# Optimization experiments

Hardware: AMD Instinct MI355X
Metric: run time of the kernel (lower is better)

## Reference

```python
import jax, jax.numpy as jnp
import numpy as np

C = 128
K = 8
B = 2
N = 8192


def setup_inputs() -> dict:
    key = jax.random.key(0)
    ks = jax.random.split(key, 7)
    feats = jax.random.normal(ks[0], (B, N, C), dtype=jnp.float32)
    coords = jax.random.normal(ks[1], (B, N, 3), dtype=jnp.float32)
    scale = 0.02
    Wq = jax.random.normal(ks[2], (C, C), dtype=jnp.float32) * scale
    Wk = jax.random.normal(ks[3], (C, C), dtype=jnp.float32) * scale
    Wv = jax.random.normal(ks[4], (C, C), dtype=jnp.float32) * scale
    Wo = jax.random.normal(ks[5], (C, C), dtype=jnp.float32) * scale
    log_gamma = jnp.log(jnp.float32(0.92))
    return {"feats": feats, "coords": coords, "Wq": Wq, "Wk": Wk,
            "Wv": Wv, "Wo": Wo, "log_gamma": log_gamma}


def _gather_neighbors(points, idx):
    # points: (B,N,C), idx: (B,N,K) -> (B,N,K,C)
    return jax.vmap(lambda p, i: p[i])(points, idx)


def _safe_norm(diff):
    # diff: (...,3) -> (...,) Euclidean norm with zero (not NaN) grad at 0
    d2 = jnp.sum(diff * diff, axis=-1)
    pos = d2 > 0
    return jnp.where(pos, jnp.sqrt(jnp.where(pos, d2, 1.0)), 0.0)


def reference(feats, coords, Wq, Wk, Wv, Wo, log_gamma):
    # nn.Linear(bias=False): y = x @ W.T with W of shape (out, in)
    q = feats @ Wq.T
    k = feats @ Wk.T
    v = feats @ Wv.T

    # KNN via dense pairwise Euclidean distance (mirrors torch.cdist + topk smallest)
    sq = jnp.sum(coords * coords, axis=-1)                      # (B,N)
    d2 = sq[:, :, None] + sq[:, None, :] - 2.0 * jnp.einsum('bnd,bmd->bnm', coords, coords)
    dist_full = jnp.sqrt(jnp.maximum(d2, 0.0))                  # (B,N,N)
    _, idx = jax.lax.top_k(-dist_full, K)                       # (B,N,K) nearest (incl. self)
    idx = jax.lax.stop_gradient(idx)

    k_neigh = _gather_neighbors(k, idx)                         # (B,N,K,C)
    v_neigh = _gather_neighbors(v, idx)                         # (B,N,K,C)
    coord_neigh = _gather_neighbors(coords, idx)                # (B,N,K,3)

    dist = _safe_norm(coords[:, :, None, :] - coord_neigh)      # (B,N,K)
    gamma_w = jnp.exp(log_gamma * dist)                         # (B,N,K)

    scores = jnp.einsum('bnc,bnkc->bnk', q, k_neigh) / (C ** 0.5)
    scores = scores * gamma_w
    weights = jax.nn.softmax(scores, axis=2)                    # (B,N,K)
    agg = jnp.einsum('bnk,bnkc->bnc', weights, v_neigh)         # (B,N,C)
    out = agg @ Wo.T
    return out
```

## Files before the change

kernel.cpp:

```cpp
#include <hip/hip_runtime.h>
#include <math.h>

#define C_DIM 128
#define KNN 8
#define NPTS 8192
#define M_TOTAL 16384
#define CHUNK 1024
#define SAMPLE 2048
#define CAND_CAP 96

typedef unsigned long long u64;

__global__ __launch_bounds__(256) void prep_and_transpose(
    const float* __restrict__ coords, float4* __restrict__ c4,
    const float* __restrict__ Wq, const float* __restrict__ Wk,
    const float* __restrict__ Wv, const float* __restrict__ Wo,
    float* __restrict__ Tq, float* __restrict__ Tk,
    float* __restrict__ Tv, float* __restrict__ To) {
  const int bid = blockIdx.x;
  const int t = threadIdx.x;
  if (bid < 64) {
    int g = bid * 256 + t;
    float x = coords[3 * g + 0];
    float y = coords[3 * g + 1];
    float z = coords[3 * g + 2];
    float s = fmaf(x, x, fmaf(y, y, z * z));
    c4[g] = make_float4(x, y, z, s);
  } else {
    int g = (bid - 64) * 256 + t;
    int mat = g >> 14;
    int j = g & 16383;
    int c = j >> 7, o = j & 127;
    const float* src = (mat == 0) ? Wq : (mat == 1) ? Wk : (mat == 2) ? Wv : Wo;
    float* dst = (mat == 0) ? Tq : (mat == 1) ? Tk : (mat == 2) ? Tv : To;
    dst[j] = src[o * C_DIM + c];
  }
}

__device__ __forceinline__ void stage_x64(
    float (*Xs)[132], const float* __restrict__ X, int row0, int t) {
  const float4* X4 = (const float4*)(X + (size_t)row0 * C_DIM);
  for (int i = t; i < 64 * 32; i += 256) {
    int r = i >> 5, c4i = i & 31;
    *(float4*)&Xs[r][c4i * 4] = X4[i];
  }
}

__global__ __launch_bounds__(256) void gemm_qkv(
    const float* __restrict__ X,
    const float* __restrict__ WTq, const float* __restrict__ WTk,
    const float* __restrict__ WTv,
    float* __restrict__ Yq, float* __restrict__ Yk, float* __restrict__ Yv) {
  __shared__ float Xs[64][132];
  __shared__ float Ws[3][16][64];
  const int t = threadIdx.x;
  const int row0 = (blockIdx.x >> 1) * 64;
  const int ob = (blockIdx.x & 1) * 64;

  stage_x64(Xs, X, row0, t);

  const int r0 = (t >> 4) * 4;
  const int o0l = (t & 15) * 4;
  const int wk = t >> 4;

  float aq[4][4], ak[4][4], av[4][4];
#pragma unroll
  for (int i = 0; i < 4; ++i)
#pragma unroll
    for (int j = 0; j < 4; ++j) { aq[i][j] = 0.f; ak[i][j] = 0.f; av[i][j] = 0.f; }

  for (int kc = 0; kc < C_DIM; kc += 16) {
    __syncthreads();
    {
      const size_t gsrc = (size_t)(kc + wk) * C_DIM + ob + o0l;
      *(float4*)&Ws[0][wk][o0l] = *(const float4*)&WTq[gsrc];
      *(float4*)&Ws[1][wk][o0l] = *(const float4*)&WTk[gsrc];
      *(float4*)&Ws[2][wk][o0l] = *(const float4*)&WTv[gsrc];
    }
    __syncthreads();

#pragma unroll
    for (int c = 0; c < 16; c += 4) {
      float xs[4][4];
#pragma unroll
      for (int i = 0; i < 4; ++i) {
        float4 xv = *(const float4*)&Xs[r0 + i][kc + c];
        xs[i][0] = xv.x; xs[i][1] = xv.y; xs[i][2] = xv.z; xs[i][3] = xv.w;
      }
#pragma unroll
      for (int cc = 0; cc < 4; ++cc) {
        float4 qa = *(const float4*)&Ws[0][c + cc][o0l];
        float4 ka = *(const float4*)&Ws[1][c + cc][o0l];
        float4 va = *(const float4*)&Ws[2][c + cc][o0l];
#pragma unroll
        for (int i = 0; i < 4; ++i) {
          float x = xs[i][cc];
          aq[i][0] = fmaf(x, qa.x, aq[i][0]); aq[i][1] = fmaf(x, qa.y, aq[i][1]);
          aq[i][2] = fmaf(x, qa.z, aq[i][2]); aq[i][3] = fmaf(x, qa.w, aq[i][3]);
          ak[i][0] = fmaf(x, ka.x, ak[i][0]); ak[i][1] = fmaf(x, ka.y, ak[i][1]);
          ak[i][2] = fmaf(x, ka.z, ak[i][2]); ak[i][3] = fmaf(x, ka.w, ak[i][3]);
          av[i][0] = fmaf(x, va.x, av[i][0]); av[i][1] = fmaf(x, va.y, av[i][1]);
          av[i][2] = fmaf(x, va.z, av[i][2]); av[i][3] = fmaf(x, va.w, av[i][3]);
        }
      }
    }
  }

#pragma unroll
  for (int i = 0; i < 4; ++i) {
    const size_t yoff = (size_t)(row0 + r0 + i) * C_DIM + ob + o0l;
    *(float4*)&Yq[yoff] = make_float4(aq[i][0], aq[i][1], aq[i][2], aq[i][3]);
    *(float4*)&Yk[yoff] = make_float4(ak[i][0], ak[i][1], ak[i][2], ak[i][3]);
    *(float4*)&Yv[yoff] = make_float4(av[i][0], av[i][1], av[i][2], av[i][3]);
  }
}

__global__ __launch_bounds__(256) void gemm_xwt(
    const float* __restrict__ X, const float* __restrict__ WT,
    float* __restrict__ Y) {
  __shared__ float Xs[64][132];
  __shared__ float Ws[16][64];
  const int t = threadIdx.x;
  const int row0 = (blockIdx.x >> 1) * 64;
  const int ob = (blockIdx.x & 1) * 64;

  stage_x64(Xs, X, row0, t);

  const int r0 = (t >> 4) * 4;
  const int o0l = (t & 15) * 4;
  const int wk = t >> 4;

  float acc[4][4];
#pragma unroll
  for (int i = 0; i < 4; ++i)
#pragma unroll
    for (int j = 0; j < 4; ++j) acc[i][j] = 0.0f;

  for (int kc = 0; kc < C_DIM; kc += 16) {
    __syncthreads();
    *(float4*)&Ws[wk][o0l] =
        *(const float4*)&WT[(size_t)(kc + wk) * C_DIM + ob + o0l];
    __syncthreads();

#pragma unroll
    for (int c = 0; c < 16; c += 4) {
      float xs[4][4];
#pragma unroll
      for (int i = 0; i < 4; ++i) {
        float4 xv = *(const float4*)&Xs[r0 + i][kc + c];
        xs[i][0] = xv.x; xs[i][1] = xv.y; xs[i][2] = xv.z; xs[i][3] = xv.w;
      }
#pragma unroll
      for (int cc = 0; cc < 4; ++cc) {
        float4 wa = *(const float4*)&Ws[c + cc][o0l];
#pragma unroll
        for (int i = 0; i < 4; ++i) {
          float x = xs[i][cc];
          acc[i][0] = fmaf(x, wa.x, acc[i][0]); acc[i][1] = fmaf(x, wa.y, acc[i][1]);
          acc[i][2] = fmaf(x, wa.z, acc[i][2]); acc[i][3] = fmaf(x, wa.w, acc[i][3]);
        }
      }
    }
  }

#pragma unroll
  for (int i = 0; i < 4; ++i) {
    float* yrow = Y + (size_t)(row0 + r0 + i) * C_DIM + ob + o0l;
    *(float4*)yrow = make_float4(acc[i][0], acc[i][1], acc[i][2], acc[i][3]);
  }
}

__device__ __forceinline__ u64 wave_min_u64(u64 x) {
#pragma unroll
  for (int off = 32; off > 0; off >>= 1) {
    u64 o = __shfl_xor(x, off, 64);
    x = (o < x) ? o : x;
  }
  return x;
}

__device__ __forceinline__ float wave_8th_of_top2(float u0, float u1) {
  float m = 0.0f;
#pragma unroll
  for (int r = 0; r < KNN; ++r) {
    m = u0;
#pragma unroll
    for (int off = 32; off > 0; off >>= 1) {
      float o = __shfl_xor(m, off, 64);
      m = fminf(m, o);
    }
    bool mine = (u0 == m);
    u0 = mine ? u1 : u0;
    u1 = mine ? INFINITY : u1;
  }
  return m;
}

__global__ __launch_bounds__(256) void knn_attn(
    const float4* __restrict__ c4,
    const float* __restrict__ q, const float* __restrict__ k,
    const float* __restrict__ v, const float* __restrict__ log_gamma_p,
    float* __restrict__ agg) {
  __shared__ float4 pts[CHUNK];
  __shared__ u64 cand[4][CAND_CAP];

  const int t = threadIdx.x;
  const int wave = t >> 6;
  const int lane = t & 63;
  const int qi = blockIdx.x * 4 + wave;
  const int b = qi >> 13;
  const int n = qi & (NPTS - 1);
  const int base = b * NPTS;

  const float4 qp = c4[base + n];
  const u64 lmask = (1ull << lane) - 1ull;

  float m1 = INFINITY, m2 = INFINITY;
  const float4* cb = c4 + base;
#pragma unroll 4
  for (int it = 0; it < SAMPLE / 64; ++it) {
    const float4 p = cb[it * 64 + lane];
    float dot = fmaf(qp.x, p.x, fmaf(qp.y, p.y, qp.z * p.z));
    float d2 = fmaxf(qp.w + p.w - 2.0f * dot, 0.0f);
    float h = fmaxf(m1, d2); m1 = fminf(m1, d2); m2 = fminf(m2, h);
  }
  const float tau = wave_8th_of_top2(m1, m2);

  int cnt = 0;
  for (int ch = 0; ch < NPTS / CHUNK; ++ch) {
    __syncthreads();
    for (int i = t; i < CHUNK; i += 256) pts[i] = c4[base + ch * CHUNK + i];
    __syncthreads();

#pragma unroll
    for (int it = 0; it < CHUNK / 128; ++it) {
      const int ml = it * 128 + lane;
      const float4 pa = pts[ml];
      const float4 pb = pts[ml + 64];
      float dota = fmaf(qp.x, pa.x, fmaf(qp.y, pa.y, qp.z * pa.z));
      float dotb = fmaf(qp.x, pb.x, fmaf(qp.y, pb.y, qp.z * pb.z));
      float d2a = fmaxf(qp.w + pa.w - 2.0f * dota, 0.0f);
      float d2b = fmaxf(qp.w + pb.w - 2.0f * dotb, 0.0f);
      bool ga = d2a <= tau;
      bool gb = d2b <= tau;
      u64 mska = __ballot(ga);
      u64 mskb = __ballot(gb);
      if (mska | mskb) {
        const unsigned ia = (unsigned)(ch * CHUNK + ml);
        if (ga) {
          int pos = cnt + (int)__popcll(mska & lmask);
          if (pos < CAND_CAP)
            cand[wave][pos] = ((u64)__float_as_uint(d2a) << 32) | ia;
        }
        cnt += (int)__popcll(mska);
        if (gb) {
          int pos = cnt + (int)__popcll(mskb & lmask);
          if (pos < CAND_CAP)
            cand[wave][pos] = ((u64)__float_as_uint(d2b) << 32) | (ia + 64);
        }
        cnt += (int)__popcll(mskb);
      }
    }
  }

  const int m_ = (cnt < CAND_CAP) ? cnt : CAND_CAP;
  u64 a = (lane < m_) ? cand[wave][lane] : ~0ull;
  u64 bb = (lane + 64 < m_) ? cand[wave][lane + 64] : ~0ull;
  u64 k0 = (a < bb) ? a : bb, k1 = (a < bb) ? bb : a;
  int ni_[KNN];
#pragma unroll
  for (int r = 0; r < KNN; ++r) {
    u64 mm = wave_min_u64(k0);
    ni_[r] = (int)(unsigned)(mm & 0xFFFFFFFFu);
    if (k0 == mm) { k0 = k1; k1 = ~0ull; }
  }

  const float lg = *log_gamma_p;
  const size_t qrow = (size_t)(base + n) * C_DIM;
  const float qv0 = q[qrow + lane];
  const float qv1 = q[qrow + lane + 64];

  float score[KNN];
#pragma unroll
  for (int j = 0; j < KNN; ++j) {
    const int mj = ni_[j];
    const size_t krow = (size_t)(base + mj) * C_DIM;
    float p = fmaf(qv1, k[krow + lane + 64], qv0 * k[krow + lane]);
#pragma unroll
    for (int off = 32; off > 0; off >>= 1) p += __shfl_xor(p, off, 64);
    const float4 pm = c4[base + mj];
    float dx = qp.x - pm.x, dy = qp.y - pm.y, dz = qp.z - pm.z;
    float d2p = fmaf(dx, dx, fmaf(dy, dy, dz * dz));
    float dist = d2p > 0.0f ? sqrtf(d2p) : 0.0f;
    float gw = expf(lg * dist);
    score[j] = (p / 11.313708498984761f) * gw;
  }

  float mx = score[0];
#pragma unroll
  for (int j = 1; j < KNN; ++j) mx = fmaxf(mx, score[j]);
  float w[KNN]; float sum = 0.0f;
#pragma unroll
  for (int j = 0; j < KNN; ++j) { w[j] = expf(score[j] - mx); sum += w[j]; }
#pragma unroll
  for (int j = 0; j < KNN; ++j) w[j] = w[j] / sum;

  float a0 = 0.0f, a1 = 0.0f;
#pragma unroll
  for (int j = 0; j < KNN; ++j) {
    const size_t vrow = (size_t)(base + ni_[j]) * C_DIM;
    a0 = fmaf(w[j], v[vrow + lane], a0);
    a1 = fmaf(w[j], v[vrow + lane + 64], a1);
  }
  agg[qrow + lane] = a0;
  agg[qrow + lane + 64] = a1;
}

extern "C" void kernel_launch(void* const* d_in, const int* in_sizes, int n_in,
                              void* d_out, int out_size, void* d_ws, size_t ws_size,
                              hipStream_t stream) {
  const float* feats  = (const float*)d_in[0];
  const float* coords = (const float*)d_in[1];
  const float* Wq     = (const float*)d_in[2];
  const float* Wk     = (const float*)d_in[3];
  const float* Wv     = (const float*)d_in[4];
  const float* Wo     = (const float*)d_in[5];
  const float* lg     = (const float*)d_in[6];
  float* out = (float*)d_out;

  float* ws = (float*)d_ws;
  const size_t ROWS = (size_t)M_TOTAL * C_DIM;
  float*  q   = ws;
  float*  k   = ws + ROWS;
  float*  v   = ws + 2 * ROWS;
  float4* c4  = (float4*)(ws + 3 * ROWS);
  float*  WTq = ws + 3 * ROWS + 4 * (size_t)M_TOTAL;
  float*  WTk = WTq + C_DIM * C_DIM;
  float*  WTv = WTk + C_DIM * C_DIM;
  float*  WTo = WTv + C_DIM * C_DIM;
  float*  agg = q;

  prep_and_transpose<<<320, 256, 0, stream>>>(coords, c4, Wq, Wk, Wv, Wo,
                                              WTq, WTk, WTv, WTo);
  gemm_qkv<<<M_TOTAL / 32, 256, 0, stream>>>(feats, WTq, WTk, WTv, q, k, v);
  knn_attn<<<M_TOTAL / 4, 256, 0, stream>>>(c4, q, k, v, lg, agg);
  gemm_xwt<<<M_TOTAL / 32, 256, 0, stream>>>(agg, WTo, out);
}
```

Before: 193.6 us.

## Compute QKV projection with bf16 MFMA instead of FP32 FMA GEMM

Replaces the scalar FP32 QKV GEMM with a kernel that converts feats and the Q/K/V weights to bf16 and uses 16x16x32 bf16 MFMA instructions, with 64-row tiles per block. The prep kernel now emits bf16 copies of Wq/Wk/Wv in their original (out,in) layout and transposes only Wo. This targets the compute cost of the projection GEMM. It lowers the precision of q/k/v, which can shift scores and possibly KNN-attention outputs beyond tolerance. Weight B-fragments are read straight from global memory rather than staged in LDS.

```diff
diff --git a/kernel.cpp b/kernel.cpp
--- a/kernel.cpp
+++ b/kernel.cpp
@@ -10,13 +10,21 @@
 #define CAND_CAP 96
 
 typedef unsigned long long u64;
-
-__global__ __launch_bounds__(256) void prep_and_transpose(
+typedef __attribute__((ext_vector_type(8))) short bf16x8;
+typedef __attribute__((ext_vector_type(4))) float f32x4;
+
+__device__ __forceinline__ short f2bf(float f) {
+  unsigned u = __float_as_uint(f);
+  unsigned r = (u + 0x7FFFu + ((u >> 16) & 1u)) >> 16;
+  return (short)r;
+}
+
+__global__ __launch_bounds__(256) void prep_all(
     const float* __restrict__ coords, float4* __restrict__ c4,
     const float* __restrict__ Wq, const float* __restrict__ Wk,
     const float* __restrict__ Wv, const float* __restrict__ Wo,
-    float* __restrict__ Tq, float* __restrict__ Tk,
-    float* __restrict__ Tv, float* __restrict__ To) {
+    float* __restrict__ To,
+    short* __restrict__ Wqb, short* __restrict__ Wkb, short* __restrict__ Wvb) {
   const int bid = blockIdx.x;
   const int t = threadIdx.x;
   if (bid < 64) {
@@ -26,14 +34,88 @@
     float z = coords[3 * g + 2];
     float s = fmaf(x, x, fmaf(y, y, z * z));
     c4[g] = make_float4(x, y, z, s);
+  } else if (bid < 128) {
+    int j = (bid - 64) * 256 + t;
+    int c = j >> 7, o = j & 127;
+    To[j] = Wo[o * C_DIM + c];
   } else {
-    int g = (bid - 64) * 256 + t;
+    int g = (bid - 128) * 256 + t;
     int mat = g >> 14;
     int j = g & 16383;
-    int c = j >> 7, o = j & 127;
-    const float* src = (mat == 0) ? Wq : (mat == 1) ? Wk : (mat == 2) ? Wv : Wo;
-    float* dst = (mat == 0) ? Tq : (mat == 1) ? Tk : (mat == 2) ? Tv : To;
-    dst[j] = src[o * C_DIM + c];
+    const float* src = (mat == 0) ? Wq : (mat == 1) ? Wk : Wv;
+    short* dst = (mat == 0) ? Wqb : (mat == 1) ? Wkb : Wvb;
+    dst[j] = f2bf(src[j]);
+  }
+}
+
+__global__ __launch_bounds__(256) void gemm_qkv_mfma(
+    const float* __restrict__ X,
+    const short* __restrict__ Wqb, const short* __restrict__ Wkb,
+    const short* __restrict__ Wvb,
+    float* __restrict__ Yq, float* __restrict__ Yk, float* __restrict__ Yv) {
+  __shared__ short As[64][136];
+  const int t = threadIdx.x;
+  const int wave = t >> 6;
+  const int lane = t & 63;
+  const int row0 = blockIdx.x * 64;
+
+  const float4* X4 = (const float4*)(X + (size_t)row0 * C_DIM);
+  for (int i = t; i < 64 * 32; i += 256) {
+    int r = i >> 5, c = i & 31;
+    float4 v = X4[i];
+    short4 s = make_short4(f2bf(v.x), f2bf(v.y), f2bf(v.z), f2bf(v.w));
+    *(short4*)&As[r][c * 4] = s;
+  }
+  __syncthreads();
+
+  const int wm = wave >> 1;
+  const int wn = wave & 1;
+  const int l15 = lane & 15;
+  const int koff = (lane >> 4) * 8;
+  const int arow = wm * 32 + l15;
+
+  f32x4 acc[3][2][4];
+#pragma unroll
+  for (int m = 0; m < 3; ++m)
+#pragma unroll
+    for (int i = 0; i < 2; ++i)
+#pragma unroll
+      for (int j = 0; j < 4; ++j) acc[m][i][j] = (f32x4){0.f, 0.f, 0.f, 0.f};
+
+  const short* Wb[3] = {Wqb, Wkb, Wvb};
+
+#pragma unroll
+  for (int kk = 0; kk < C_DIM; kk += 32) {
+    bf16x8 a0 = *(const bf16x8*)&As[arow][kk + koff];
+    bf16x8 a1 = *(const bf16x8*)&As[arow + 16][kk + koff];
+#pragma unroll
+    for (int m = 0; m < 3; ++m) {
+#pragma unroll
+      for (int fn = 0; fn < 4; ++fn) {
+        const int n = wn * 64 + fn * 16 + l15;
+        bf16x8 b = *(const bf16x8*)&Wb[m][n * C_DIM + kk + koff];
+        acc[m][0][fn] =
+            __builtin_amdgcn_mfma_f32_16x16x32_bf16(a0, b, acc[m][0][fn], 0, 0, 0);
+        acc[m][1][fn] =
+            __builtin_amdgcn_mfma_f32_16x16x32_bf16(a1, b, acc[m][1][fn], 0, 0, 0);
+      }
+    }
+  }
+
+  float* Y[3] = {Yq, Yk, Yv};
+#pragma unroll
+  for (int m = 0; m < 3; ++m) {
+#pragma unroll
+    for (int fm = 0; fm < 2; ++fm) {
+      const int rbase = row0 + wm * 32 + fm * 16 + (lane >> 4) * 4;
+#pragma unroll
+      for (int fn = 0; fn < 4; ++fn) {
+        const int col = wn * 64 + fn * 16 + l15;
+#pragma unroll
+        for (int j = 0; j < 4; ++j)
+          Y[m][(size_t)(rbase + j) * C_DIM + col] = acc[m][fm][fn][j];
+      }
+    }
   }
 }
 
@@ -43,75 +125,6 @@
   for (int i = t; i < 64 * 32; i += 256) {
     int r = i >> 5, c4i = i & 31;
     *(float4*)&Xs[r][c4i * 4] = X4[i];
-  }
-}
-
-__global__ __launch_bounds__(256) void gemm_qkv(
-    const float* __restrict__ X,
-    const float* __restrict__ WTq, const float* __restrict__ WTk,
-    const float* __restrict__ WTv,
-    float* __restrict__ Yq, float* __restrict__ Yk, float* __restrict__ Yv) {
-  __shared__ float Xs[64][132];
-  __shared__ float Ws[3][16][64];
-  const int t = threadIdx.x;
-  const int row0 = (blockIdx.x >> 1) * 64;
-  const int ob = (blockIdx.x & 1) * 64;
-
-  stage_x64(Xs, X, row0, t);
-
-  const int r0 = (t >> 4) * 4;
-  const int o0l = (t & 15) * 4;
-  const int wk = t >> 4;
-
-  float aq[4][4], ak[4][4], av[4][4];
-#pragma unroll
-  for (int i = 0; i < 4; ++i)
-#pragma unroll
-    for (int j = 0; j < 4; ++j) { aq[i][j] = 0.f; ak[i][j] = 0.f; av[i][j] = 0.f; }
-
-  for (int kc = 0; kc < C_DIM; kc += 16) {
-    __syncthreads();
-    {
-      const size_t gsrc = (size_t)(kc + wk) * C_DIM + ob + o0l;
-      *(float4*)&Ws[0][wk][o0l] = *(const float4*)&WTq[gsrc];
-      *(float4*)&Ws[1][wk][o0l] = *(const float4*)&WTk[gsrc];
-      *(float4*)&Ws[2][wk][o0l] = *(const float4*)&WTv[gsrc];
-    }
-    __syncthreads();
-
-#pragma unroll
-    for (int c = 0; c < 16; c += 4) {
-      float xs[4][4];
-#pragma unroll
-      for (int i = 0; i < 4; ++i) {
-        float4 xv = *(const float4*)&Xs[r0 + i][kc + c];
-        xs[i][0] = xv.x; xs[i][1] = xv.y; xs[i][2] = xv.z; xs[i][3] = xv.w;
-      }
-#pragma unroll
-      for (int cc = 0; cc < 4; ++cc) {
-        float4 qa = *(const float4*)&Ws[0][c + cc][o0l];
-        float4 ka = *(const float4*)&Ws[1][c + cc][o0l];
-        float4 va = *(const float4*)&Ws[2][c + cc][o0l];
-#pragma unroll
-        for (int i = 0; i < 4; ++i) {
-          float x = xs[i][cc];
-          aq[i][0] = fmaf(x, qa.x, aq[i][0]); aq[i][1] = fmaf(x, qa.y, aq[i][1]);
-          aq[i][2] = fmaf(x, qa.z, aq[i][2]); aq[i][3] = fmaf(x, qa.w, aq[i][3]);
-          ak[i][0] = fmaf(x, ka.x, ak[i][0]); ak[i][1] = fmaf(x, ka.y, ak[i][1]);
-          ak[i][2] = fmaf(x, ka.z, ak[i][2]); ak[i][3] = fmaf(x, ka.w, ak[i][3]);
-          av[i][0] = fmaf(x, va.x, av[i][0]); av[i][1] = fmaf(x, va.y, av[i][1]);
-          av[i][2] = fmaf(x, va.z, av[i][2]); av[i][3] = fmaf(x, va.w, av[i][3]);
-        }
-      }
-    }
-  }
-
-#pragma unroll
-  for (int i = 0; i < 4; ++i) {
-    const size_t yoff = (size_t)(row0 + r0 + i) * C_DIM + ob + o0l;
-    *(float4*)&Yq[yoff] = make_float4(aq[i][0], aq[i][1], aq[i][2], aq[i][3]);
-    *(float4*)&Yk[yoff] = make_float4(ak[i][0], ak[i][1], ak[i][2], ak[i][3]);
-    *(float4*)&Yv[yoff] = make_float4(av[i][0], av[i][1], av[i][2], av[i][3]);
   }
 }
 
@@ -334,15 +347,16 @@
   float*  k   = ws + ROWS;
   float*  v   = ws + 2 * ROWS;
   float4* c4  = (float4*)(ws + 3 * ROWS);
-  float*  WTq = ws + 3 * ROWS + 4 * (size_t)M_TOTAL;
-  float*  WTk = WTq + C_DIM * C_DIM;
-  float*  WTv = WTk + C_DIM * C_DIM;
-  float*  WTo = WTv + C_DIM * C_DIM;
+  float*  WTo = ws + 3 * ROWS + 4 * (size_t)M_TOTAL;
+  short*  Wqb = (short*)(WTo + C_DIM * C_DIM);
+  short*  Wkb = Wqb + C_DIM * C_DIM;
+  short*  Wvb = Wkb + C_DIM * C_DIM;
   float*  agg = q;
 
-  prep_and_transpose<<<320, 256, 0, stream>>>(coords, c4, Wq, Wk, Wv, Wo,
-                                              WTq, WTk, WTv, WTo);
-  gemm_qkv<<<M_TOTAL / 32, 256, 0, stream>>>(feats, WTq, WTk, WTv, q, k, v);
+  prep_all<<<320, 256, 0, stream>>>(coords, c4, Wq, Wk, Wv, Wo,
+                                    WTo, Wqb, Wkb, Wvb);
+  gemm_qkv_mfma<<<M_TOTAL / 64, 256, 0, stream>>>(feats, Wqb, Wkb, Wvb,
+                                                  q, k, v);
   knn_attn<<<M_TOTAL / 4, 256, 0, stream>>>(c4, q, k, v, lg, agg);
   gemm_xwt<<<M_TOTAL / 32, 256, 0, stream>>>(agg, WTo, out);
 }
```

After: 183.2 us. 1.06x faster.
